# Kernel optimization log

Measured on AMD Instinct MI355X. Metric: run time of the kernel, lower is better.

The kernel has to match this reference:

```python
import jax, jax.numpy as jnp
import numpy as np

N, E, C_IN, C_OUT, G = 100000, 1250000, 64, 64, 64
H = 2 * C_OUT  # hidden width of conv1 output


def _lin(k, out_d, in_d, scale=0.05):
    kw, kb = jax.random.split(k)
    return (jax.random.normal(kw, (out_d, in_d), jnp.float32) * scale,
            jax.random.normal(kb, (out_d,), jnp.float32) * scale)


def setup_inputs() -> dict:
    key = jax.random.key(0)
    ks = jax.random.split(key, 12)
    x = jax.random.normal(ks[0], (N, C_IN), jnp.float32)
    edge_index = jax.random.randint(ks[1], (2, E), 0, N, jnp.int64)
    batch = jnp.sort(jax.random.randint(ks[2], (N,), 0, G, jnp.int64))
    # GraphConv layer 1: lin_rel (with bias) on aggregated msgs, lin_root (no bias) on x
    w1_rel, b1_rel = _lin(ks[3], H, C_IN)
    w1_root = jax.random.normal(ks[4], (H, C_IN), jnp.float32) * 0.05
    # GraphConv layer 2
    w2_rel, b2_rel = _lin(ks[5], C_OUT, H)
    w2_root = jax.random.normal(ks[6], (C_OUT, H), jnp.float32) * 0.05
    # encoder_S: out_channels -> 8 -> 4 -> 1
    es_w1, es_b1 = _lin(ks[7], 8, C_OUT)
    es_w2, es_b2 = _lin(ks[8], 4, 8)
    es_w3, es_b3 = _lin(ks[9], 1, 4)
    # decoder: 1 -> 4 -> 8 -> out_channels (input dim fixed from buggy 2 to 1)
    d_w1, d_b1 = _lin(ks[10], 4, 1)
    d_w2, d_b2 = _lin(ks[11], 8, 4)
    d_w3, d_b3 = _lin(jax.random.fold_in(key, 99), C_OUT, 8)
    return dict(x=x, edge_index=edge_index, batch=batch,
                w1_rel=w1_rel, b1_rel=b1_rel, w1_root=w1_root,
                w2_rel=w2_rel, b2_rel=b2_rel, w2_root=w2_root,
                es_w1=es_w1, es_b1=es_b1, es_w2=es_w2, es_b2=es_b2,
                es_w3=es_w3, es_b3=es_b3,
                d_w1=d_w1, d_b1=d_b1, d_w2=d_w2, d_b2=d_b2,
                d_w3=d_w3, d_b3=d_b3)


def reference(x, edge_index, batch,
              w1_rel, b1_rel, w1_root,
              w2_rel, b2_rel, w2_root,
              es_w1, es_b1, es_w2, es_b2, es_w3, es_b3,
              d_w1, d_b1, d_w2, d_b2, d_w3, d_b3):
    src, dst = edge_index[0], edge_index[1]
    # GraphConv 1: sum-aggregate source feats into targets, then rel+root linears
    agg1 = jax.ops.segment_sum(x[src], dst, num_segments=N)  # [N, C_IN]
    h1 = jax.nn.relu(agg1 @ w1_rel.T + b1_rel + x @ w1_root.T)  # [N, H]
    # GraphConv 2
    agg2 = jax.ops.segment_sum(h1[src], dst, num_segments=N)
    h2 = jax.nn.relu(agg2 @ w2_rel.T + b2_rel + h1 @ w2_root.T)  # [N, C_OUT]
    # global mean pool over graphs
    counts = jax.ops.segment_sum(jnp.ones((N,), h2.dtype), batch, num_segments=G)
    h3 = jax.ops.segment_sum(h2, batch, num_segments=G) / jnp.maximum(counts, 1.0)[:, None]  # [G, C_OUT]
    # encoder_S MLP -> z
    z = jax.nn.relu(h3 @ es_w1.T + es_b1)
    z = jax.nn.relu(z @ es_w2.T + es_b2)
    z = z @ es_w3.T + es_b3  # [G, 1]
    # decoder MLP -> x_
    x_ = jax.nn.relu(z @ d_w1.T + d_b1)
    x_ = jax.nn.relu(x_ @ d_w2.T + d_b2)
    x_ = x_ @ d_w3.T + d_b3  # [G, C_OUT]
    return h3, x_
```

## Files before the change

### kernel.cpp

```cpp
#include <hip/hip_runtime.h>
#include <stdint.h>

#define NN 100000
#define EE 1250000
#define NBUCK 196
#define CHUNK 4096
#define NCHUNK ((EE + CHUNK - 1) / CHUNK)
#define PSLICE 24
#define XB_NB ((NN * 64 / 4 + 255) / 256)

typedef __attribute__((ext_vector_type(8))) short short8;
typedef __attribute__((ext_vector_type(4))) float f32x4;

__device__ inline ushort f2bf(float f) {
  union { float f; uint32_t u; } v; v.f = f;
  uint32_t r = v.u + 0x7FFF + ((v.u >> 16) & 1);
  return (ushort)(r >> 16);
}
__device__ inline float bf2f(ushort h) {
  union { uint32_t u; float f; } v; v.u = ((uint32_t)h) << 16;
  return v.f;
}

__global__ __launch_bounds__(256) void kfront(const float* __restrict__ w1_rel,
                                              const float* __restrict__ w1_root,
                                              const float* __restrict__ w2_rel,
                                              const float* __restrict__ w2_root,
                                              const float* __restrict__ x,
                                              const int* __restrict__ dstI,
                                              ushort* __restrict__ WF,
                                              ushort* __restrict__ xb,
                                              int* __restrict__ histG) {
  __shared__ int h[NBUCK];
  int t = threadIdx.x;
  int blk = blockIdx.x;
  if (blk < 32) {
    int idx = blk * 256 + t;
    if (idx < 8192) {
      int j = idx & 7, l = (idx >> 3) & 63, ts = idx >> 9;
      {
        int s = ts & 1, tt = ts >> 1;
        int o = tt * 16 + (l & 15), k = s * 32 + (l >> 4) * 8 + j;
        WF[idx] = f2bf(w1_rel[o * 64 + k]);
        WF[8192 + idx] = f2bf(w1_root[o * 64 + k]);
      }
      {
        int s = ts & 3, tt = ts >> 2;
        int o = tt * 16 + (l & 15), k = s * 32 + (l >> 4) * 8 + j;
        WF[16384 + idx] = f2bf(w2_rel[o * 128 + k]);
        WF[24576 + idx] = f2bf(w2_root[o * 128 + k]);
      }
    }
  } else if (blk < 32 + XB_NB) {
    int i = ((blk - 32) * 256 + t) * 4;
    if (i < NN * 64) {
      float4 v = *reinterpret_cast<const float4*>(x + i);
      ushort o[4] = {f2bf(v.x), f2bf(v.y), f2bf(v.z), f2bf(v.w)};
      *reinterpret_cast<uint2*>(xb + i) = *reinterpret_cast<uint2*>(o);
    }
  } else {
    int c = blk - 32 - XB_NB;
    if (t < NBUCK) h[t] = 0;
    __syncthreads();
    int cb = c * CHUNK;
    int cc = EE - cb; if (cc > CHUNK) cc = CHUNK;
    for (int i = t; i < cc; i += 256) atomicAdd(&h[dstI[cb + i] >> 9], 1);
    __syncthreads();
    if (t < NBUCK) histG[c * NBUCK + t] = h[t];
  }
}

__global__ __launch_bounds__(512) void kscan2d(const int* __restrict__ histG,
                                               int* __restrict__ relG,
                                               int* __restrict__ bucketTotal) {
  __shared__ int sm[512];
  int b = blockIdx.x;
  int t = threadIdx.x;
  int v = (t < NCHUNK) ? histG[t * NBUCK + b] : 0;
  sm[t] = v;
  __syncthreads();
  for (int d = 1; d < 512; d <<= 1) {
    int u = (t >= d) ? sm[t - d] : 0;
    __syncthreads();
    sm[t] += u;
    __syncthreads();
  }
  if (t < NCHUNK) relG[t * NBUCK + b] = sm[t] - v;
  if (t == 511) bucketTotal[b] = sm[511];
}

__global__ __launch_bounds__(256) void kscan196(const int* __restrict__ bucketTotal,
                                                int* __restrict__ bucketStart) {
  __shared__ int ss[256];
  int t = threadIdx.x;
  int v = (t < NBUCK) ? bucketTotal[t] : 0;
  ss[t] = v;
  __syncthreads();
  for (int d = 1; d < 256; d <<= 1) {
    int u = (t >= d) ? ss[t - d] : 0;
    __syncthreads();
    ss[t] += u;
    __syncthreads();
  }
  if (t < NBUCK) bucketStart[t] = ss[t] - v;
  if (t == NBUCK - 1) bucketStart[NBUCK] = ss[t];
}

__global__ __launch_bounds__(256) void kbinA2(const int* __restrict__ srcI,
                                              const int* __restrict__ dstI,
                                              const int* __restrict__ histG,
                                              const int* __restrict__ relG,
                                              const int* __restrict__ bucketStart,
                                              uint32_t* __restrict__ pairsG) {
  __shared__ uint32_t pko[CHUNK];
  __shared__ int ss[256];
  __shared__ int ex[NBUCK + 1];
  __shared__ int cur[NBUCK];
  __shared__ int gb[NBUCK];
  int t = threadIdx.x;
  int cb = blockIdx.x * CHUNK;
  int cc = EE - cb; if (cc > CHUNK) cc = CHUNK;

  int v = (t < NBUCK) ? histG[blockIdx.x * NBUCK + t] : 0;
  ss[t] = v;
  __syncthreads();
  for (int d = 1; d < 256; d <<= 1) {
    int u = (t >= d) ? ss[t - d] : 0;
    __syncthreads();
    ss[t] += u;
    __syncthreads();
  }
  if (t < NBUCK) {
    ex[t] = ss[t] - v;
    cur[t] = ss[t] - v;
    gb[t] = bucketStart[t] + relG[blockIdx.x * NBUCK + t];
  }
  if (t == NBUCK - 1) ex[NBUCK] = ss[t];
  __syncthreads();
  for (int i = t; i < cc; i += 256) {
    int d = dstI[cb + i];
    int s = srcI[cb + i];
    int b = d >> 9;
    int p = atomicAdd(&cur[b], 1);
    pko[p] = (uint32_t)s | ((uint32_t)(d & 511) << 17);
  }
  __syncthreads();
  if (t < NBUCK) {
    int base = ex[t], cnt = ex[t + 1] - base, g0 = gb[t];
    for (int j = 0; j < cnt; ++j) pairsG[g0 + j] = pko[base + j];
  }
}

__global__ __launch_bounds__(256) void kbinB(const uint32_t* __restrict__ pairsG,
                                             const int* __restrict__ bucketStart,
                                             int* __restrict__ starts,
                                             int* __restrict__ esrc) {
  __shared__ int hist[512];
  __shared__ int ex2[512];
  __shared__ int part[256];
  int t = threadIdx.x;
  int b = blockIdx.x;
  int nbase = b << 9;
  int base = bucketStart[b];
  int ecnt = bucketStart[b + 1] - base;

  hist[t] = 0; hist[t + 256] = 0;
  __syncthreads();
  for (int i = t; i < ecnt; i += 256) atomicAdd(&hist[pairsG[base + i] >> 17], 1);
  __syncthreads();
  int a = hist[2 * t], c = hist[2 * t + 1];
  part[t] = a + c;
  __syncthreads();
  for (int d = 1; d < 256; d <<= 1) {
    int u = (t >= d) ? part[t - d] : 0;
    __syncthreads();
    part[t] += u;
    __syncthreads();
  }
  int pex = part[t] - (a + c);
  ex2[2 * t] = pex;
  ex2[2 * t + 1] = pex + a;
  __syncthreads();
  for (int n = t; n < 512; n += 256) {
    int node = nbase + n;
    if (node < NN) starts[node] = base + ex2[n];
  }
  if (b == NBUCK - 1 && t == 0) starts[NN] = EE;
  for (int n = t; n < 512; n += 256) hist[n] = ex2[n];
  __syncthreads();
  for (int i = t; i < ecnt; i += 256) {
    uint32_t p = pairsG[base + i];
    int dl = p >> 17;
    int s = p & 0x1FFFF;
    int lp = atomicAdd(&hist[dl], 1);
    esrc[base + lp] = s;
  }
}

#define GATHER_CORE(featb)                                                         \
  float a0 = 0.f, a1 = 0.f, a2 = 0.f, a3 = 0.f;                                    \
  const ushort* fb = (featb) + 4 * lq;                                             \
  int i = b;                                                                       \
  {                                                                                \
    int s0 = 0, s1 = 0, s2 = 0, s3 = 0, s4 = 0, s5 = 0, s6 = 0, s7 = 0;            \
    bool have = (i + 8 <= e);                                                      \
    if (have) {                                                                    \
      s0 = esrc[i];     s1 = esrc[i + 1]; s2 = esrc[i + 2]; s3 = esrc[i + 3];      \
      s4 = esrc[i + 4]; s5 = esrc[i + 5]; s6 = esrc[i + 6]; s7 = esrc[i + 7];      \
    }                                                                              \
    while (have) {                                                                 \
      uint2 u0 = *(const uint2*)(fb + (size_t)s0 * 64);                            \
      uint2 u1 = *(const uint2*)(fb + (size_t)s1 * 64);                            \
      uint2 u2 = *(const uint2*)(fb + (size_t)s2 * 64);                            \
      uint2 u3 = *(const uint2*)(fb + (size_t)s3 * 64);                            \
      uint2 u4 = *(const uint2*)(fb + (size_t)s4 * 64);                            \
      uint2 u5 = *(const uint2*)(fb + (size_t)s5 * 64);                            \
      uint2 u6 = *(const uint2*)(fb + (size_t)s6 * 64);                            \
      uint2 u7 = *(const uint2*)(fb + (size_t)s7 * 64);                            \
      i += 8;                                                                      \
      have = (i + 8 <= e);                                                         \
      if (have) {                                                                  \
        s0 = esrc[i];     s1 = esrc[i + 1]; s2 = esrc[i + 2]; s3 = esrc[i + 3];    \
        s4 = esrc[i + 4]; s5 = esrc[i + 5]; s6 = esrc[i + 6]; s7 = esrc[i + 7];    \
      }                                                                            \
      a0 += bf2f((ushort)u0.x) + bf2f((ushort)u1.x) + bf2f((ushort)u2.x) +         \
            bf2f((ushort)u3.x) + bf2f((ushort)u4.x) + bf2f((ushort)u5.x) +         \
            bf2f((ushort)u6.x) + bf2f((ushort)u7.x);                               \
      a1 += bf2f((ushort)(u0.x >> 16)) + bf2f((ushort)(u1.x >> 16)) +              \
            bf2f((ushort)(u2.x >> 16)) + bf2f((ushort)(u3.x >> 16)) +              \
            bf2f((ushort)(u4.x >> 16)) + bf2f((ushort)(u5.x >> 16)) +              \
            bf2f((ushort)(u6.x >> 16)) + bf2f((ushort)(u7.x >> 16));               \
      a2 += bf2f((ushort)u0.y) + bf2f((ushort)u1.y) + bf2f((ushort)u2.y) +         \
            bf2f((ushort)u3.y) + bf2f((ushort)u4.y) + bf2f((ushort)u5.y) +         \
            bf2f((ushort)u6.y) + bf2f((ushort)u7.y);                               \
      a3 += bf2f((ushort)(u0.y >> 16)) + bf2f((ushort)(u1.y >> 16)) +              \
            bf2f((ushort)(u2.y >> 16)) + bf2f((ushort)(u3.y >> 16)) +              \
            bf2f((ushort)(u4.y >> 16)) + bf2f((ushort)(u5.y >> 16)) +              \
            bf2f((ushort)(u6.y >> 16)) + bf2f((ushort)(u7.y >> 16));               \
    }                                                                              \
  }                                                                                \
  if (i + 4 <= e) {                                                                \
    int s0 = esrc[i], s1 = esrc[i + 1], s2 = esrc[i + 2], s3 = esrc[i + 3];        \
    uint2 u0 = *(const uint2*)(fb + (size_t)s0 * 64);                              \
    uint2 u1 = *(const uint2*)(fb + (size_t)s1 * 64);                              \
    uint2 u2 = *(const uint2*)(fb + (size_t)s2 * 64);                              \
    uint2 u3 = *(const uint2*)(fb + (size_t)s3 * 64);                              \
    a0 += bf2f((ushort)u0.x) + bf2f((ushort)u1.x) + bf2f((ushort)u2.x) + bf2f((ushort)u3.x); \
    a1 += bf2f((ushort)(u0.x >> 16)) + bf2f((ushort)(u1.x >> 16)) +                \
          bf2f((ushort)(u2.x >> 16)) + bf2f((ushort)(u3.x >> 16));                 \
    a2 += bf2f((ushort)u0.y) + bf2f((ushort)u1.y) + bf2f((ushort)u2.y) + bf2f((ushort)u3.y); \
    a3 += bf2f((ushort)(u0.y >> 16)) + bf2f((ushort)(u1.y >> 16)) +                \
          bf2f((ushort)(u2.y >> 16)) + bf2f((ushort)(u3.y >> 16));                 \
    i += 4;                                                                        \
  }                                                                                \
  if (i + 2 <= e) {                                                                \
    int s0 = esrc[i], s1 = esrc[i + 1];                                            \
    uint2 u0 = *(const uint2*)(fb + (size_t)s0 * 64);                              \
    uint2 u1 = *(const uint2*)(fb + (size_t)s1 * 64);                              \
    a0 += bf2f((ushort)u0.x) + bf2f((ushort)u1.x);                                 \
    a1 += bf2f((ushort)(u0.x >> 16)) + bf2f((ushort)(u1.x >> 16));                 \
    a2 += bf2f((ushort)u0.y) + bf2f((ushort)u1.y);                                 \
    a3 += bf2f((ushort)(u0.y >> 16)) + bf2f((ushort)(u1.y >> 16));                 \
    i += 2;                                                                        \
  }                                                                                \
  if (i < e) {                                                                     \
    int s0 = esrc[i];                                                              \
    uint2 u0 = *(const uint2*)(fb + (size_t)s0 * 64);                              \
    a0 += bf2f((ushort)u0.x); a1 += bf2f((ushort)(u0.x >> 16));                    \
    a2 += bf2f((ushort)u0.y); a3 += bf2f((ushort)(u0.y >> 16));                    \
  }

__global__ __launch_bounds__(256) void kgatherQ(const ushort* __restrict__ featb,
                                                const int* __restrict__ starts,
                                                const int* __restrict__ esrc,
                                                ushort* __restrict__ outb) {
  int w = (blockIdx.x * 256 + threadIdx.x) >> 4;
  if (w >= NN) return;
  int lq = threadIdx.x & 15;
  int b = starts[w], e = starts[w + 1];
  GATHER_CORE(featb)
  uint2 o;
  o.x = (uint32_t)f2bf(a0) | ((uint32_t)f2bf(a1) << 16);
  o.y = (uint32_t)f2bf(a2) | ((uint32_t)f2bf(a3) << 16);
  *(uint2*)(outb + (size_t)w * 64 + 4 * lq) = o;
}

__global__ __launch_bounds__(256) void kgh2Q(const ushort* __restrict__ featb,
                                             const int* __restrict__ starts,
                                             const int* __restrict__ esrc,
                                             const ushort* __restrict__ r2b,
                                             const float* __restrict__ b2v,
                                             ushort* __restrict__ h2b) {
  int w = (blockIdx.x * 256 + threadIdx.x) >> 4;
  if (w >= NN) return;
  int lq = threadIdx.x & 15;
  int b = starts[w], e = starts[w + 1];
  GATHER_CORE(featb)
  uint2 ru = *(const uint2*)(r2b + (size_t)w * 64 + 4 * lq);
  float4 bias = *(const float4*)(b2v + 4 * lq);
  float v0 = fmaxf(a0 + bf2f((ushort)ru.x) + bias.x, 0.f);
  float v1 = fmaxf(a1 + bf2f((ushort)(ru.x >> 16)) + bias.y, 0.f);
  float v2 = fmaxf(a2 + bf2f((ushort)ru.y) + bias.z, 0.f);
  float v3 = fmaxf(a3 + bf2f((ushort)(ru.y >> 16)) + bias.w, 0.f);
  uint2 o;
  o.x = (uint32_t)f2bf(v0) | ((uint32_t)f2bf(v1) << 16);
  o.y = (uint32_t)f2bf(v2) | ((uint32_t)f2bf(v3) << 16);
  *(uint2*)(h2b + (size_t)w * 64 + 4 * lq) = o;
}

__global__ __launch_bounds__(256) void kfused(const ushort* __restrict__ xb,
                                              const ushort* __restrict__ aggb,
                                              const ushort* __restrict__ WF,
                                              const float* __restrict__ b1,
                                              ushort* __restrict__ y,
                                              ushort* __restrict__ r2b) {
  __shared__ __align__(16) char hT[32768];
  int t = threadIdx.x, l = t & 63, wv = t >> 6;
  int n0 = blockIdx.x * 128 + wv * 32;
  int row = l & 15;
  int kg = l >> 4;
  int nr0 = n0 + row;      if (nr0 > NN - 1) nr0 = NN - 1;
  int nr1 = n0 + 16 + row; if (nr1 > NN - 1) nr1 = NN - 1;

  short8 aA0[2], aX0[2], aA1[2], aX1[2];
  {
    const ushort* ap0 = aggb + (size_t)nr0 * 64 + kg * 8;
    aA0[0] = *(const short8*)(ap0);
    aA0[1] = *(const short8*)(ap0 + 32);
    const ushort* xp0 = xb + (size_t)nr0 * 64 + kg * 8;
    aX0[0] = *(const short8*)(xp0);
    aX0[1] = *(const short8*)(xp0 + 32);
    const ushort* ap1 = aggb + (size_t)nr1 * 64 + kg * 8;
    aA1[0] = *(const short8*)(ap1);
    aA1[1] = *(const short8*)(ap1 + 32);
    const ushort* xp1 = xb + (size_t)nr1 * 64 + kg * 8;
    aX1[0] = *(const short8*)(xp1);
    aX1[1] = *(const short8*)(xp1 + 32);
  }

  const ushort* wf1rel = WF;
  const ushort* wf1root = WF + 8192;
  char* base0 = hT + wv * 8192;
  char* base1 = base0 + 4096;

#pragma unroll
  for (int tt = 0; tt < 8; ++tt) {
    f32x4 acc0 = {0.f, 0.f, 0.f, 0.f};
    f32x4 acc1 = {0.f, 0.f, 0.f, 0.f};
#pragma unroll
    for (int s = 0; s < 2; ++s) {
      short8 br = *(const short8*)(wf1rel + ((size_t)(tt * 2 + s) * 64 + l) * 8);
      short8 bo = *(const short8*)(wf1root + ((size_t)(tt * 2 + s) * 64 + l) * 8);
      acc0 = __builtin_amdgcn_mfma_f32_16x16x32_bf16(aA0[s], br, acc0, 0, 0, 0);
      acc0 = __builtin_amdgcn_mfma_f32_16x16x32_bf16(aX0[s], bo, acc0, 0, 0, 0);
      acc1 = __builtin_amdgcn_mfma_f32_16x16x32_bf16(aA1[s], br, acc1, 0, 0, 0);
      acc1 = __builtin_amdgcn_mfma_f32_16x16x32_bf16(aX1[s], bo, acc1, 0, 0, 0);
    }
    float bias = b1[tt * 16 + row];
#pragma unroll
    for (int r = 0; r < 4; ++r) {
      int nl = kg * 4 + r;
      int off = nl * 256 + (tt * 16 + row) * 2;
      off ^= (nl & 7) << 4;
      *(ushort*)(base0 + off) = f2bf(fmaxf(acc0[r] + bias, 0.f));
      *(ushort*)(base1 + off) = f2bf(fmaxf(acc1[r] + bias, 0.f));
    }
  }
  __syncthreads();

  short8 aH0[4], aH1[4];
#pragma unroll
  for (int s = 0; s < 4; ++s) {
    int off = row * 256 + s * 64 + kg * 16;
    off ^= (row & 7) << 4;
    aH0[s] = *(const short8*)(base0 + off);
    aH1[s] = *(const short8*)(base1 + off);
  }

  const ushort* wf2rel = WF + 16384;
  const ushort* wf2root = WF + 24576;
#pragma unroll
  for (int tt = 0; tt < 4; ++tt) {
    f32x4 accY0 = {0.f, 0.f, 0.f, 0.f};
    f32x4 accR0 = {0.f, 0.f, 0.f, 0.f};
    f32x4 accY1 = {0.f, 0.f, 0.f, 0.f};
    f32x4 accR1 = {0.f, 0.f, 0.f, 0.f};
#pragma unroll
    for (int s = 0; s < 4; ++s) {
      short8 br = *(const short8*)(wf2rel + ((size_t)(tt * 4 + s) * 64 + l) * 8);
      short8 bo = *(const short8*)(wf2root + ((size_t)(tt * 4 + s) * 64 + l) * 8);
      accY0 = __builtin_amdgcn_mfma_f32_16x16x32_bf16(aH0[s], br, accY0, 0, 0, 0);
      accR0 = __builtin_amdgcn_mfma_f32_16x16x32_bf16(aH0[s], bo, accR0, 0, 0, 0);
      accY1 = __builtin_amdgcn_mfma_f32_16x16x32_bf16(aH1[s], br, accY1, 0, 0, 0);
      accR1 = __builtin_amdgcn_mfma_f32_16x16x32_bf16(aH1[s], bo, accR1, 0, 0, 0);
    }
#pragma unroll
    for (int r = 0; r < 4; ++r) {
      int nd0 = n0 + kg * 4 + r;
      int nd1 = nd0 + 16;
      if (nd0 < NN) {
        y[(size_t)nd0 * 64 + tt * 16 + row] = f2bf(accY0[r]);
        r2b[(size_t)nd0 * 64 + tt * 16 + row] = f2bf(accR0[r]);
      }
      if (nd1 < NN) {
        y[(size_t)nd1 * 64 + tt * 16 + row] = f2bf(accY1[r]);
        r2b[(size_t)nd1 * 64 + tt * 16 + row] = f2bf(accR1[r]);
      }
    }
  }
}

__global__ __launch_bounds__(256) void kpoolpart(const ushort* __restrict__ h2b,
                                                 const int* __restrict__ batch,
                                                 float* __restrict__ poolP) {
  __shared__ int gbs[2];
  __shared__ float part[4][64];
  int g = blockIdx.x / PSLICE, sl = blockIdx.x % PSLICE;
  int t = threadIdx.x;
  if (t < 2) {
    int target = g + t;
    int lo = 0, hi = NN;
    while (lo < hi) { int m = (lo + hi) >> 1; if (batch[m] < target) lo = m + 1; else hi = m; }
    gbs[t] = lo;
  }
  __syncthreads();
  int n0 = gbs[0], len = gbs[1] - n0;
  int lo = n0 + (int)((long)len * sl / PSLICE);
  int hi = n0 + (int)((long)len * (sl + 1) / PSLICE);
  int ch = t & 63, sub = t >> 6;
  float acc = 0.f;
  int n = lo + sub;
  for (; n + 12 < hi; n += 16) {
    float v0 = bf2f(h2b[(size_t)n * 64 + ch]);
    float v1 = bf2f(h2b[(size_t)(n + 4) * 64 + ch]);
    float v2 = bf2f(h2b[(size_t)(n + 8) * 64 + ch]);
    float v3 = bf2f(h2b[(size_t)(n + 12) * 64 + ch]);
    acc += (v0 + v1) + (v2 + v3);
  }
  for (; n < hi; n += 4) acc += bf2f(h2b[(size_t)n * 64 + ch]);
  part[sub][ch] = acc;
  __syncthreads();
  if (t < 64)
    poolP[(size_t)blockIdx.x * 64 + t] = part[0][t] + part[1][t] + part[2][t] + part[3][t];
}

__global__ __launch_bounds__(64) void kfinal3(
    const float* __restrict__ poolP, const int* __restrict__ batch,
    const float* __restrict__ es_w1, const float* __restrict__ es_b1,
    const float* __restrict__ es_w2, const float* __restrict__ es_b2,
    const float* __restrict__ es_w3, const float* __restrict__ es_b3,
    const float* __restrict__ d_w1, const float* __restrict__ d_b1,
    const float* __restrict__ d_w2, const float* __restrict__ d_b2,
    const float* __restrict__ d_w3, const float* __restrict__ d_b3,
    float* __restrict__ out) {
  __shared__ float h3[64];
  __shared__ float z1s[8];
  __shared__ float t2s[8];
  __shared__ int gbs[2];
  int g = blockIdx.x;
  int l = threadIdx.x;
  if (l < 2) {
    int target = g + l;
    int lo = 0, hi = NN;
    while (lo < hi) { int m = (lo + hi) >> 1; if (batch[m] < target) lo = m + 1; else hi = m; }
    gbs[l] = lo;
  }
  float s = 0.f;
#pragma unroll
  for (int k = 0; k < PSLICE; ++k) s += poolP[(size_t)(g * PSLICE + k) * 64 + l];
  __syncthreads();
  float c = fmaxf((float)(gbs[1] - gbs[0]), 1.f);
  float h = s / c;
  h3[l] = h;
  out[g * 64 + l] = h;
  __syncthreads();
  if (l < 8) {
    float a = es_b1[l];
#pragma unroll
    for (int k = 0; k < 64; ++k) a += es_w1[l * 64 + k] * h3[k];
    z1s[l] = fmaxf(a, 0.f);
  }
  __syncthreads();
  if (l == 0) {
    float z2[4];
#pragma unroll
    for (int j = 0; j < 4; ++j) {
      float a = es_b2[j];
#pragma unroll
      for (int k = 0; k < 8; ++k) a += es_w2[j * 8 + k] * z1s[k];
      z2[j] = fmaxf(a, 0.f);
    }
    float z = es_b3[0];
#pragma unroll
    for (int k = 0; k < 4; ++k) z += es_w3[k] * z2[k];
    float t1[4];
#pragma unroll
    for (int j = 0; j < 4; ++j) t1[j] = fmaxf(d_w1[j] * z + d_b1[j], 0.f);
#pragma unroll
    for (int j = 0; j < 8; ++j) {
      float a = d_b2[j];
#pragma unroll
      for (int k = 0; k < 4; ++k) a += d_w2[j * 4 + k] * t1[k];
      t2s[j] = fmaxf(a, 0.f);
    }
  }
  __syncthreads();
  float a = d_b3[l];
#pragma unroll
  for (int k = 0; k < 8; ++k) a += d_w3[l * 8 + k] * t2s[k];
  out[4096 + g * 64 + l] = a;
}

extern "C" void kernel_launch(void* const* d_in, const int* in_sizes, int n_in,
                              void* d_out, int out_size, void* d_ws, size_t ws_size,
                              hipStream_t stream) {
  const float* x = (const float*)d_in[0];
  const int* ei = (const int*)d_in[1];
  const int* srcI = ei;
  const int* dstI = ei + EE;
  const int* batch = (const int*)d_in[2];
  const float* w1_rel = (const float*)d_in[3];
  const float* b1_rel = (const float*)d_in[4];
  const float* w1_root = (const float*)d_in[5];
  const float* w2_rel = (const float*)d_in[6];
  const float* b2_rel = (const float*)d_in[7];
  const float* w2_root = (const float*)d_in[8];
  const float* es_w1 = (const float*)d_in[9];
  const float* es_b1 = (const float*)d_in[10];
  const float* es_w2 = (const float*)d_in[11];
  const float* es_b2 = (const float*)d_in[12];
  const float* es_w3 = (const float*)d_in[13];
  const float* es_b3 = (const float*)d_in[14];
  const float* d_w1 = (const float*)d_in[15];
  const float* d_b1 = (const float*)d_in[16];
  const float* d_w2 = (const float*)d_in[17];
  const float* d_b2 = (const float*)d_in[18];
  const float* d_w3 = (const float*)d_in[19];
  const float* d_b3 = (const float*)d_in[20];

  ushort* xb = (ushort*)d_ws;
  ushort* aggb = xb + (size_t)NN * 64;
  ushort* yb = aggb + (size_t)NN * 64;
  ushort* r2b = yb + (size_t)NN * 64;
  ushort* h2b = r2b + (size_t)NN * 64;
  ushort* WF = h2b + (size_t)NN * 64;
  float* poolP = (float*)(WF + 32768);
  int* starts = (int*)(poolP + 64 * PSLICE * 64);
  int* histG = starts + NN + 1;
  int* relG = histG + NCHUNK * NBUCK;
  int* bucketTotal = relG + NCHUNK * NBUCK;
  int* bucketStart = bucketTotal + NBUCK;
  uint32_t* pairsG = (uint32_t*)(bucketStart + NBUCK + 1);
  int* esrc = (int*)(pairsG + EE);
  float* out = (float*)d_out;

  kfront<<<32 + XB_NB + NCHUNK, 256, 0, stream>>>(w1_rel, w1_root, w2_rel, w2_root,
                                                  x, dstI, WF, xb, histG);
  kscan2d<<<NBUCK, 512, 0, stream>>>(histG, relG, bucketTotal);
  kscan196<<<1, 256, 0, stream>>>(bucketTotal, bucketStart);
  kbinA2<<<NCHUNK, 256, 0, stream>>>(srcI, dstI, histG, relG, bucketStart, pairsG);
  kbinB<<<NBUCK, 256, 0, stream>>>(pairsG, bucketStart, starts, esrc);
  kgatherQ<<<(NN * 16 + 255) / 256, 256, 0, stream>>>(xb, starts, esrc, aggb);
  kfused<<<(NN + 127) / 128, 256, 0, stream>>>(xb, aggb, WF, b1_rel, yb, r2b);
  kgh2Q<<<(NN * 16 + 255) / 256, 256, 0, stream>>>(yb, starts, esrc, r2b, b2_rel, h2b);
  kpoolpart<<<64 * PSLICE, 256, 0, stream>>>(h2b, batch, poolP);
  kfinal3<<<64, 64, 0, stream>>>(poolP, batch, es_w1, es_b1, es_w2, es_b2, es_w3, es_b3,
                                 d_w1, d_b1, d_w2, d_b2, d_w3, d_b3, out);
}
```

Before: 139.6 us.

## Widen gather loads to 16 bytes per lane and fold bucket scan into consumers

The two neighbour-gather kernels now use 8 lanes per node, each loading a uint4 (8 bf16 values) instead of 16 lanes loading uint2. This halves the thread count and the esrc index loads per edge, and issues wider memory requests. Separately, the single-block bucket-prefix kernel is removed and each kbinA2/kbinB block recomputes the 196-entry scan locally, saving one launch but adding redundant scan work per block.

```diff
diff --git a/kernel.cpp b/kernel.cpp
--- a/kernel.cpp
+++ b/kernel.cpp
@@ -89,31 +89,15 @@
   if (t == 511) bucketTotal[b] = sm[511];
 }
 
-__global__ __launch_bounds__(256) void kscan196(const int* __restrict__ bucketTotal,
-                                                int* __restrict__ bucketStart) {
-  __shared__ int ss[256];
-  int t = threadIdx.x;
-  int v = (t < NBUCK) ? bucketTotal[t] : 0;
-  ss[t] = v;
-  __syncthreads();
-  for (int d = 1; d < 256; d <<= 1) {
-    int u = (t >= d) ? ss[t - d] : 0;
-    __syncthreads();
-    ss[t] += u;
-    __syncthreads();
-  }
-  if (t < NBUCK) bucketStart[t] = ss[t] - v;
-  if (t == NBUCK - 1) bucketStart[NBUCK] = ss[t];
-}
-
 __global__ __launch_bounds__(256) void kbinA2(const int* __restrict__ srcI,
                                               const int* __restrict__ dstI,
                                               const int* __restrict__ histG,
                                               const int* __restrict__ relG,
-                                              const int* __restrict__ bucketStart,
+                                              const int* __restrict__ bucketTotal,
                                               uint32_t* __restrict__ pairsG) {
   __shared__ uint32_t pko[CHUNK];
   __shared__ int ss[256];
+  __shared__ int bsL[NBUCK];
   __shared__ int ex[NBUCK + 1];
   __shared__ int cur[NBUCK];
   __shared__ int gb[NBUCK];
@@ -121,6 +105,19 @@
   int cb = blockIdx.x * CHUNK;
   int cc = EE - cb; if (cc > CHUNK) cc = CHUNK;
 
+  {
+    int bv = (t < NBUCK) ? bucketTotal[t] : 0;
+    ss[t] = bv;
+    __syncthreads();
+    for (int d = 1; d < 256; d <<= 1) {
+      int u = (t >= d) ? ss[t - d] : 0;
+      __syncthreads();
+      ss[t] += u;
+      __syncthreads();
+    }
+    if (t < NBUCK) bsL[t] = ss[t] - bv;
+    __syncthreads();
+  }
   int v = (t < NBUCK) ? histG[blockIdx.x * NBUCK + t] : 0;
   ss[t] = v;
   __syncthreads();
@@ -133,7 +130,7 @@
   if (t < NBUCK) {
     ex[t] = ss[t] - v;
     cur[t] = ss[t] - v;
-    gb[t] = bucketStart[t] + relG[blockIdx.x * NBUCK + t];
+    gb[t] = bsL[t] + relG[blockIdx.x * NBUCK + t];
   }
   if (t == NBUCK - 1) ex[NBUCK] = ss[t];
   __syncthreads();
@@ -152,17 +149,31 @@
 }
 
 __global__ __launch_bounds__(256) void kbinB(const uint32_t* __restrict__ pairsG,
-                                             const int* __restrict__ bucketStart,
+                                             const int* __restrict__ bucketTotal,
                                              int* __restrict__ starts,
                                              int* __restrict__ esrc) {
   __shared__ int hist[512];
   __shared__ int ex2[512];
   __shared__ int part[256];
+  __shared__ int baseS;
   int t = threadIdx.x;
   int b = blockIdx.x;
   int nbase = b << 9;
-  int base = bucketStart[b];
-  int ecnt = bucketStart[b + 1] - base;
+  {
+    int bv = (t < NBUCK) ? bucketTotal[t] : 0;
+    part[t] = bv;
+    __syncthreads();
+    for (int d = 1; d < 256; d <<= 1) {
+      int u = (t >= d) ? part[t - d] : 0;
+      __syncthreads();
+      part[t] += u;
+      __syncthreads();
+    }
+    if (t == b) baseS = part[t] - bv;
+    __syncthreads();
+  }
+  int base = baseS;
+  int ecnt = bucketTotal[b];
 
   hist[t] = 0; hist[t + 256] = 0;
   __syncthreads();
@@ -197,9 +208,16 @@
   }
 }
 
-#define GATHER_CORE(featb)                                                         \
-  float a0 = 0.f, a1 = 0.f, a2 = 0.f, a3 = 0.f;                                    \
-  const ushort* fb = (featb) + 4 * lq;                                             \
+#define ACC8(u)                                                                    \
+  a0 += bf2f((ushort)(u).x); a1 += bf2f((ushort)((u).x >> 16));                    \
+  a2 += bf2f((ushort)(u).y); a3 += bf2f((ushort)((u).y >> 16));                    \
+  a4 += bf2f((ushort)(u).z); a5 += bf2f((ushort)((u).z >> 16));                    \
+  a6 += bf2f((ushort)(u).w); a7 += bf2f((ushort)((u).w >> 16));
+
+#define GATHER_CORE8(featb)                                                        \
+  float a0 = 0.f, a1 = 0.f, a2 = 0.f, a3 = 0.f,                                    \
+        a4 = 0.f, a5 = 0.f, a6 = 0.f, a7 = 0.f;                                    \
+  const ushort* fb = (featb) + 8 * lg;                                             \
   int i = b;                                                                       \
   {                                                                                \
     int s0 = 0, s1 = 0, s2 = 0, s3 = 0, s4 = 0, s5 = 0, s6 = 0, s7 = 0;            \
@@ -209,80 +227,60 @@
       s4 = esrc[i + 4]; s5 = esrc[i + 5]; s6 = esrc[i + 6]; s7 = esrc[i + 7];      \
     }                                                                              \
     while (have) {                                                                 \
-      uint2 u0 = *(const uint2*)(fb + (size_t)s0 * 64);                            \
-      uint2 u1 = *(const uint2*)(fb + (size_t)s1 * 64);                            \
-      uint2 u2 = *(const uint2*)(fb + (size_t)s2 * 64);                            \
-      uint2 u3 = *(const uint2*)(fb + (size_t)s3 * 64);                            \
-      uint2 u4 = *(const uint2*)(fb + (size_t)s4 * 64);                            \
-      uint2 u5 = *(const uint2*)(fb + (size_t)s5 * 64);                            \
-      uint2 u6 = *(const uint2*)(fb + (size_t)s6 * 64);                            \
-      uint2 u7 = *(const uint2*)(fb + (size_t)s7 * 64);                            \
+      uint4 u0 = *(const uint4*)(fb + (size_t)s0 * 64);                            \
+      uint4 u1 = *(const uint4*)(fb + (size_t)s1 * 64);                            \
+      uint4 u2 = *(const uint4*)(fb + (size_t)s2 * 64);                            \
+      uint4 u3 = *(const uint4*)(fb + (size_t)s3 * 64);                            \
+      uint4 u4 = *(const uint4*)(fb + (size_t)s4 * 64);                            \
+      uint4 u5 = *(const uint4*)(fb + (size_t)s5 * 64);                            \
+      uint4 u6 = *(const uint4*)(fb + (size_t)s6 * 64);                            \
+      uint4 u7 = *(const uint4*)(fb + (size_t)s7 * 64);                            \
       i += 8;                                                                      \
       have = (i + 8 <= e);                                                         \
       if (have) {                                                                  \
         s0 = esrc[i];     s1 = esrc[i + 1]; s2 = esrc[i + 2]; s3 = esrc[i + 3];    \
         s4 = esrc[i + 4]; s5 = esrc[i + 5]; s6 = esrc[i + 6]; s7 = esrc[i + 7];    \
       }                                                                            \
-      a0 += bf2f((ushort)u0.x) + bf2f((ushort)u1.x) + bf2f((ushort)u2.x) +         \
-            bf2f((ushort)u3.x) + bf2f((ushort)u4.x) + bf2f((ushort)u5.x) +         \
-            bf2f((ushort)u6.x) + bf2f((ushort)u7.x);                               \
-      a1 += bf2f((ushort)(u0.x >> 16)) + bf2f((ushort)(u1.x >> 16)) +              \
-            bf2f((ushort)(u2.x >> 16)) + bf2f((ushort)(u3.x >> 16)) +              \
-            bf2f((ushort)(u4.x >> 16)) + bf2f((ushort)(u5.x >> 16)) +              \
-            bf2f((ushort)(u6.x >> 16)) + bf2f((ushort)(u7.x >> 16));               \
-      a2 += bf2f((ushort)u0.y) + bf2f((ushort)u1.y) + bf2f((ushort)u2.y) +         \
-            bf2f((ushort)u3.y) + bf2f((ushort)u4.y) + bf2f((ushort)u5.y) +         \
-            bf2f((ushort)u6.y) + bf2f((ushort)u7.y);                               \
-      a3 += bf2f((ushort)(u0.y >> 16)) + bf2f((ushort)(u1.y >> 16)) +              \
-            bf2f((ushort)(u2.y >> 16)) + bf2f((ushort)(u3.y >> 16)) +              \
-            bf2f((ushort)(u4.y >> 16)) + bf2f((ushort)(u5.y >> 16)) +              \
-            bf2f((ushort)(u6.y >> 16)) + bf2f((ushort)(u7.y >> 16));               \
+      ACC8(u0) ACC8(u1) ACC8(u2) ACC8(u3) ACC8(u4) ACC8(u5) ACC8(u6) ACC8(u7)      \
     }                                                                              \
   }                                                                                \
   if (i + 4 <= e) {                                                                \
     int s0 = esrc[i], s1 = esrc[i + 1], s2 = esrc[i + 2], s3 = esrc[i + 3];        \
-    uint2 u0 = *(const uint2*)(fb + (size_t)s0 * 64);                              \
-    uint2 u1 = *(const uint2*)(fb + (size_t)s1 * 64);                              \
-    uint2 u2 = *(const uint2*)(fb + (size_t)s2 * 64);                              \
-    uint2 u3 = *(const uint2*)(fb + (size_t)s3 * 64);                              \
-    a0 += bf2f((ushort)u0.x) + bf2f((ushort)u1.x) + bf2f((ushort)u2.x) + bf2f((ushort)u3.x); \
-    a1 += bf2f((ushort)(u0.x >> 16)) + bf2f((ushort)(u1.x >> 16)) +                \
-          bf2f((ushort)(u2.x >> 16)) + bf2f((ushort)(u3.x >> 16));                 \
-    a2 += bf2f((ushort)u0.y) + bf2f((ushort)u1.y) + bf2f((ushort)u2.y) + bf2f((ushort)u3.y); \
-    a3 += bf2f((ushort)(u0.y >> 16)) + bf2f((ushort)(u1.y >> 16)) +                \
-          bf2f((ushort)(u2.y >> 16)) + bf2f((ushort)(u3.y >> 16));                 \
+    uint4 u0 = *(const uint4*)(fb + (size_t)s0 * 64);                              \
+    uint4 u1 = *(const uint4*)(fb + (size_t)s1 * 64);                              \
+    uint4 u2 = *(const uint4*)(fb + (size_t)s2 * 64);                              \
+    uint4 u3 = *(const uint4*)(fb + (size_t)s3 * 64);                              \
+    ACC8(u0) ACC8(u1) ACC8(u2) ACC8(u3)                                            \
     i += 4;                                                                        \
   }                                                                                \
   if (i + 2 <= e) {                                                                \
     int s0 = esrc[i], s1 = esrc[i + 1];                                            \
-    uint2 u0 = *(const uint2*)(fb + (size_t)s0 * 64);                              \
-    uint2 u1 = *(const uint2*)(fb + (size_t)s1 * 64);                              \
-    a0 += bf2f((ushort)u0.x) + bf2f((ushort)u1.x);                                 \
-    a1 += bf2f((ushort)(u0.x >> 16)) + bf2f((ushort)(u1.x >> 16));                 \
-    a2 += bf2f((ushort)u0.y) + bf2f((ushort)u1.y);                                 \
-    a3 += bf2f((ushort)(u0.y >> 16)) + bf2f((ushort)(u1.y >> 16));                 \
+    uint4 u0 = *(const uint4*)(fb + (size_t)s0 * 64);                              \
+    uint4 u1 = *(const uint4*)(fb + (size_t)s1 * 64);                              \
+    ACC8(u0) ACC8(u1)                                                              \
     i += 2;                                                                        \
   }                                                                                \
   if (i < e) {                                                                     \
     int s0 = esrc[i];                                                              \
-    uint2 u0 = *(const uint2*)(fb + (size_t)s0 * 64);                              \
-    a0 += bf2f((ushort)u0.x); a1 += bf2f((ushort)(u0.x >> 16));                    \
-    a2 += bf2f((ushort)u0.y); a3 += bf2f((ushort)(u0.y >> 16));                    \
+    uint4 u0 = *(const uint4*)(fb + (size_t)s0 * 64);                              \
+    ACC8(u0)                                                                       \
   }
 
 __global__ __launch_bounds__(256) void kgatherQ(const ushort* __restrict__ featb,
                                                 const int* __restrict__ starts,
                                                 const int* __restrict__ esrc,
                                                 ushort* __restrict__ outb) {
-  int w = (blockIdx.x * 256 + threadIdx.x) >> 4;
+  int w = (blockIdx.x * 256 + threadIdx.x) >> 3;
   if (w >= NN) return;
-  int lq = threadIdx.x & 15;
+  int lg = threadIdx.x & 7;
   int b = starts[w], e = starts[w + 1];
-  GATHER_CORE(featb)
-  uint2 o;
+  GATHER_CORE8(featb)
+  uint4 o;
   o.x = (uint32_t)f2bf(a0) | ((uint32_t)f2bf(a1) << 16);
   o.y = (uint32_t)f2bf(a2) | ((uint32_t)f2bf(a3) << 16);
-  *(uint2*)(outb + (size_t)w * 64 + 4 * lq) = o;
+  o.z = (uint32_t)f2bf(a4) | ((uint32_t)f2bf(a5) << 16);
+  o.w = (uint32_t)f2bf(a6) | ((uint32_t)f2bf(a7) << 16);
+  *(uint4*)(outb + (size_t)w * 64 + 8 * lg) = o;
 }
 
 __global__ __launch_bounds__(256) void kgh2Q(const ushort* __restrict__ featb,
@@ -291,21 +289,28 @@
                                              const ushort* __restrict__ r2b,
                                              const float* __restrict__ b2v,
                                              ushort* __restrict__ h2b) {
-  int w = (blockIdx.x * 256 + threadIdx.x) >> 4;
+  int w = (blockIdx.x * 256 + threadIdx.x) >> 3;
   if (w >= NN) return;
-  int lq = threadIdx.x & 15;
+  int lg = threadIdx.x & 7;
   int b = starts[w], e = starts[w + 1];
-  GATHER_CORE(featb)
-  uint2 ru = *(const uint2*)(r2b + (size_t)w * 64 + 4 * lq);
-  float4 bias = *(const float4*)(b2v + 4 * lq);
-  float v0 = fmaxf(a0 + bf2f((ushort)ru.x) + bias.x, 0.f);
-  float v1 = fmaxf(a1 + bf2f((ushort)(ru.x >> 16)) + bias.y, 0.f);
-  float v2 = fmaxf(a2 + bf2f((ushort)ru.y) + bias.z, 0.f);
-  float v3 = fmaxf(a3 + bf2f((ushort)(ru.y >> 16)) + bias.w, 0.f);
-  uint2 o;
+  GATHER_CORE8(featb)
+  uint4 ru = *(const uint4*)(r2b + (size_t)w * 64 + 8 * lg);
+  float4 bA = *(const float4*)(b2v + 8 * lg);
+  float4 bB = *(const float4*)(b2v + 8 * lg + 4);
+  float v0 = fmaxf(a0 + bf2f((ushort)ru.x) + bA.x, 0.f);
+  float v1 = fmaxf(a1 + bf2f((ushort)(ru.x >> 16)) + bA.y, 0.f);
+  float v2 = fmaxf(a2 + bf2f((ushort)ru.y) + bA.z, 0.f);
+  float v3 = fmaxf(a3 + bf2f((ushort)(ru.y >> 16)) + bA.w, 0.f);
+  float v4 = fmaxf(a4 + bf2f((ushort)ru.z) + bB.x, 0.f);
+  float v5 = fmaxf(a5 + bf2f((ushort)(ru.z >> 16)) + bB.y, 0.f);
+  float v6 = fmaxf(a6 + bf2f((ushort)ru.w) + bB.z, 0.f);
+  float v7 = fmaxf(a7 + bf2f((ushort)(ru.w >> 16)) + bB.w, 0.f);
+  uint4 o;
   o.x = (uint32_t)f2bf(v0) | ((uint32_t)f2bf(v1) << 16);
   o.y = (uint32_t)f2bf(v2) | ((uint32_t)f2bf(v3) << 16);
-  *(uint2*)(h2b + (size_t)w * 64 + 4 * lq) = o;
+  o.z = (uint32_t)f2bf(v4) | ((uint32_t)f2bf(v5) << 16);
+  o.w = (uint32_t)f2bf(v6) | ((uint32_t)f2bf(v7) << 16);
+  *(uint4*)(h2b + (size_t)w * 64 + 8 * lg) = o;
 }
 
 __global__ __launch_bounds__(256) void kfused(const ushort* __restrict__ xb,
@@ -549,20 +554,18 @@
   int* histG = starts + NN + 1;
   int* relG = histG + NCHUNK * NBUCK;
   int* bucketTotal = relG + NCHUNK * NBUCK;
-  int* bucketStart = bucketTotal + NBUCK;
-  uint32_t* pairsG = (uint32_t*)(bucketStart + NBUCK + 1);
+  uint32_t* pairsG = (uint32_t*)(bucketTotal + NBUCK);
   int* esrc = (int*)(pairsG + EE);
   float* out = (float*)d_out;
 
   kfront<<<32 + XB_NB + NCHUNK, 256, 0, stream>>>(w1_rel, w1_root, w2_rel, w2_root,
                                                   x, dstI, WF, xb, histG);
   kscan2d<<<NBUCK, 512, 0, stream>>>(histG, relG, bucketTotal);
-  kscan196<<<1, 256, 0, stream>>>(bucketTotal, bucketStart);
-  kbinA2<<<NCHUNK, 256, 0, stream>>>(srcI, dstI, histG, relG, bucketStart, pairsG);
-  kbinB<<<NBUCK, 256, 0, stream>>>(pairsG, bucketStart, starts, esrc);
-  kgatherQ<<<(NN * 16 + 255) / 256, 256, 0, stream>>>(xb, starts, esrc, aggb);
+  kbinA2<<<NCHUNK, 256, 0, stream>>>(srcI, dstI, histG, relG, bucketTotal, pairsG);
+  kbinB<<<NBUCK, 256, 0, stream>>>(pairsG, bucketTotal, starts, esrc);
+  kgatherQ<<<(NN * 8 + 255) / 256, 256, 0, stream>>>(xb, starts, esrc, aggb);
   kfused<<<(NN + 127) / 128, 256, 0, stream>>>(xb, aggb, WF, b1_rel, yb, r2b);
-  kgh2Q<<<(NN * 16 + 255) / 256, 256, 0, stream>>>(yb, starts, esrc, r2b, b2_rel, h2b);
+  kgh2Q<<<(NN * 8 + 255) / 256, 256, 0, stream>>>(yb, starts, esrc, r2b, b2_rel, h2b);
   kpoolpart<<<64 * PSLICE, 256, 0, stream>>>(h2b, batch, poolP);
   kfinal3<<<64, 64, 0, stream>>>(poolP, batch, es_w1, es_b1, es_w2, es_b2, es_w3, es_b3,
                                  d_w1, d_b1, d_w2, d_b2, d_w3, d_b3, out);
```

Result: faster. 135.3 us (median of 2 runs) (-3.0%).
